# Optimization experiments

Measured on AMD Instinct MI355X. Metric: run time of the kernel, lower is better.

Reference implementation:

```python
import jax, jax.numpy as jnp
import numpy as np

N = 100000
E = 200000
SD = 128   # structural_dim
CD = 768   # chemical_dim


def _linear_params(key, fan_in, fan_out):
    kw, kb = jax.random.split(key)
    bound = 1.0 / np.sqrt(fan_in)
    W = jax.random.uniform(kw, (fan_in, fan_out), jnp.float32, -bound, bound)
    b = jax.random.uniform(kb, (fan_out,), jnp.float32, -bound, bound)
    return W, b


def setup_inputs() -> dict:
    key = jax.random.key(0)
    ks = jax.random.split(key, 12)
    z = jax.random.normal(ks[0], (N, SD), jnp.float32)
    chemistry = jax.random.normal(ks[1], (N, CD), jnp.float32)
    edge = jax.random.randint(ks[2], (E, 2), 0, N, jnp.int64)
    smiles_mask = jax.random.randint(ks[3], (N,), 0, 2, jnp.int32)
    # structural_mlp: SD -> SD//2 -> 1
    sw1, sb1 = _linear_params(ks[4], SD, SD // 2)
    sw2, sb2 = _linear_params(ks[5], SD // 2, 1)
    # chemical_mlp: CD -> CD//4 -> 1
    cw1, cb1 = _linear_params(ks[6], CD, CD // 4)
    cw2, cb2 = _linear_params(ks[7], CD // 4, 1)
    # combined_mlp: SD+CD -> SD -> 1
    mw1, mb1 = _linear_params(ks[8], SD + CD, SD)
    mw2, mb2 = _linear_params(ks[9], SD, 1)
    path_weights = jnp.ones((3,), jnp.float32) / 3.0
    return dict(z=z, chemistry=chemistry, edge=edge, smiles_mask=smiles_mask,
                sw1=sw1, sb1=sb1, sw2=sw2, sb2=sb2,
                cw1=cw1, cb1=cb1, cw2=cw2, cb2=cb2,
                mw1=mw1, mb1=mb1, mw2=mw2, mb2=mb2,
                path_weights=path_weights)


def reference(z, chemistry, edge, smiles_mask,
              sw1, sb1, sw2, sb2,
              cw1, cb1, cw2, cb2,
              mw1, mb1, mw2, mb2,
              path_weights):
    src, dst = edge[:, 0], edge[:, 1]
    # per-edge gathers + elementwise products
    structural_prod = z[src] * z[dst]                    # [E, SD]
    chemical_prod = chemistry[src] * chemistry[dst]      # [E, CD]
    # three small MLPs (dropout is identity in eval mode)
    score_structural = (jax.nn.relu(structural_prod @ sw1 + sb1) @ sw2 + sb2)[:, 0]
    score_chemical = (jax.nn.relu(chemical_prod @ cw1 + cb1) @ cw2 + cb2)[:, 0]
    combined_prod = jnp.concatenate([structural_prod, chemical_prod], axis=-1)  # [E, SD+CD]
    score_combined = (jax.nn.relu(combined_prod @ mw1 + mb1) @ mw2 + mb2)[:, 0]
    # fixed learned path weights (use_gating=False)
    w = jax.nn.softmax(path_weights)
    scores = w[0] * score_structural + w[1] * score_chemical + w[2] * score_combined
    # fall back to structural-only score where chemistry is missing on either end
    mask = smiles_mask.astype(z.dtype)
    both_valid = mask[src] * mask[dst]
    return jnp.where(both_valid > 0.5, scores, score_structural)  # [E]
```

## Files before the change

### kernel.cpp

```cpp
#include <hip/hip_runtime.h>


typedef float    f32x4 __attribute__((ext_vector_type(4)));
typedef _Float16 f16x8 __attribute__((ext_vector_type(8)));
typedef _Float16 f16x4 __attribute__((ext_vector_type(4)));

#define E_EDGES 200000
#define KSTEPS  28
#define NOUT    384
#define PTOT    (KSTEPS * NOUT * 32)
#define PANEL   (NOUT * 32)

#define WS_WH    0
#define WS_B1    688128
#define WS_W2    (688128 + 1536)
#define WS_CONST (688128 + 3072)

__global__ __launch_bounds__(256) void prep_kernel(
    const float* __restrict__ sw1, const float* __restrict__ sb1,
    const float* __restrict__ sw2, const float* __restrict__ sb2,
    const float* __restrict__ cw1, const float* __restrict__ cb1,
    const float* __restrict__ cw2, const float* __restrict__ cb2,
    const float* __restrict__ mw1, const float* __restrict__ mb1,
    const float* __restrict__ mw2, const float* __restrict__ mb2,
    const float* __restrict__ pw,  const int* __restrict__ edge_i32,
    _Float16* __restrict__ wh,
    float* __restrict__ b1cat, float* __restrict__ w2cat,
    float* __restrict__ consts)
{
  const int idx = blockIdx.x * 256 + threadIdx.x;
  if (idx < PTOT) {
    const int p  = idx / PANEL;
    const int r  = idx % PANEL;
    const int n  = r >> 5;
    const int kk = r & 31;
    const int k  = p * 32 + kk;
    float v;
    if (n < 64)       v = (k < 128)  ? sw1[k * 64 + n] : 0.0f;
    else if (n < 256) v = (k >= 128) ? cw1[(size_t)(k - 128) * 192 + (n - 64)] : 0.0f;
    else              v = mw1[(size_t)k * 128 + (n - 256)];
    wh[idx] = (_Float16)v;
  } else if (idx < PTOT + NOUT) {
    const int j = idx - PTOT;
    float b, w;
    if (j < 64)       { b = sb1[j];       w = sw2[j]; }
    else if (j < 256) { b = cb1[j - 64];  w = cw2[j - 64]; }
    else              { b = mb1[j - 256]; w = mw2[j - 256]; }
    b1cat[j] = b;
    w2cat[j] = w;
  } else if (idx == PTOT + NOUT) {
    const float p0 = pw[0], p1 = pw[1], p2 = pw[2];
    const float mx = fmaxf(p0, fmaxf(p1, p2));
    const float e0 = __expf(p0 - mx), e1 = __expf(p1 - mx), e2 = __expf(p2 - mx);
    const float inv = 1.0f / (e0 + e1 + e2);
    const float w0 = e0 * inv, w1 = e1 * inv, w2v = e2 * inv;
    consts[0] = w0; consts[1] = w1; consts[2] = w2v;
    consts[3] = w0 * sb2[0] + w1 * cb2[0] + w2v * mb2[0];
    consts[4] = sb2[0];
    unsigned o = 0;
    for (int i = 0; i < 64; ++i) o |= (unsigned)edge_i32[2 * i + 1];
    consts[5] = (o == 0u) ? 1.0f : 0.0f;
  }
}

#define FMA2(ACC, AH, AL, B)                                              \
  ACC = __builtin_amdgcn_mfma_f32_16x16x32_f16(AH, B, ACC, 0, 0, 0);      \
  ACC = __builtin_amdgcn_mfma_f32_16x16x32_f16(AL, B, ACC, 0, 0, 0);

__global__ __launch_bounds__(256, 3) void decoder_main(
    const float* __restrict__ z, const float* __restrict__ chem,
    const int* __restrict__ edge, const int* __restrict__ mask,
    const _Float16* __restrict__ wh,
    const float* __restrict__ b1cat, const float* __restrict__ w2cat,
    const float* __restrict__ consts, float* __restrict__ out)
{
  __shared__ _Float16 Ah[2][32][40];
  __shared__ _Float16 Al[2][32][40];
  __shared__ int   srcL[32];
  __shared__ int   dstL[32];
  __shared__ float validL[32];
  __shared__ float scoreW[4][32];

  const int tid  = threadIdx.x;
  const int lane = tid & 63;
  const int wv   = tid >> 6;
  const int li   = lane & 15;
  const int q    = lane >> 4;
  const int base = blockIdx.x * 32;

  if (tid < 32) {
    const int e = base + tid;
    int s_, d_;
    if (consts[5] > 0.5f) { s_ = edge[4 * e]; d_ = edge[4 * e + 2]; }
    else                  { s_ = edge[2 * e]; d_ = edge[2 * e + 1]; }
    srcL[tid] = s_;
    dstL[tid] = d_;
    validL[tid] = (mask[s_] != 0 && mask[d_] != 0) ? 1.0f : 0.0f;
  }
  __syncthreads();

  const int m  = tid >> 3;
  const int kc = (tid & 7) << 2;
  const float* zs = z    + (size_t)srcL[m] * 128 + kc;
  const float* zd = z    + (size_t)dstL[m] * 128 + kc;
  const float* cs = chem + (size_t)srcL[m] * 768 + kc;
  const float* cd = chem + (size_t)dstL[m] * 768 + kc;

#define GLOAD(T, A, B)                                      \
  if ((T) < 4) {                                            \
    A = *(const f32x4*)(zs + (T) * 32);                     \
    B = *(const f32x4*)(zd + (T) * 32);                     \
  } else {                                                  \
    A = *(const f32x4*)(cs + ((T) - 4) * 32);               \
    B = *(const f32x4*)(cd + ((T) - 4) * 32);               \
  }

#define STAGE(BUF, PA, PB)                                  \
  {                                                         \
    f16x4 h_, l_;                                           \
    _Pragma("unroll")                                       \
    for (int j = 0; j < 4; ++j) {                           \
      const float p_ = (PA)[j] * (PB)[j];                   \
      const _Float16 hh = (_Float16)p_;                     \
      h_[j] = hh;                                           \
      l_[j] = (_Float16)(p_ - (float)hh);                   \
    }                                                       \
    *(f16x4*)&Ah[BUF][m][kc] = h_;                          \
    *(f16x4*)&Al[BUF][m][kc] = l_;                          \
  }

#define BFRAG(S, TI) \
  (*(const f16x8*)(wh + (size_t)(S) * PANEL + ((TI) * 16 + li) * 32 + q * 8))

#define AFRAGS(BUF, A0H, A0L, A1H, A1L)                     \
  A0H = *(const f16x8*)&Ah[BUF][li][q * 8];                 \
  A0L = *(const f16x8*)&Al[BUF][li][q * 8];                 \
  A1H = *(const f16x8*)&Ah[BUF][16 + li][q * 8];            \
  A1L = *(const f16x8*)&Al[BUF][16 + li][q * 8];

  const float w0c = consts[0], w1c = consts[1], w2c = consts[2];

  float part[2][4];
#pragma unroll
  for (int mt = 0; mt < 2; ++mt)
#pragma unroll
    for (int r = 0; r < 4; ++r) part[mt][r] = 0.0f;

#define RETIRE(ACC, TI, MT, WVALID, WINVALID)                              \
  {                                                                        \
    const int col = (TI) * 16 + li;                                        \
    const float b1 = b1cat[col];                                           \
    const float w2 = w2cat[col];                                           \
    _Pragma("unroll")                                                      \
    for (int r = 0; r < 4; ++r) {                                          \
      const float vld = validL[(MT) * 16 + q * 4 + r];                     \
      const float a = (WINVALID) + vld * ((WVALID) - (WINVALID));          \
      part[MT][r] += a * fmaxf((ACC)[r] + b1, 0.0f) * w2;                  \
    }                                                                      \
  }

  const int tS  = wv;
  const int tH0 = 4 + 3 * wv;
  const int tC0 = 16 + 2 * wv;

  {
    f32x4 a0, b0;
    GLOAD(0, a0, b0)
    STAGE(0, a0, b0)
  }
  f32x4 gca, gcb;
  GLOAD(1, gca, gcb)
  __syncthreads();

  f32x4 accS[2], accC[2][2];
  accS[0] = (f32x4){0.f, 0.f, 0.f, 0.f};
  accS[1] = (f32x4){0.f, 0.f, 0.f, 0.f};
#pragma unroll
  for (int t = 0; t < 2; ++t) {
    accC[t][0] = (f32x4){0.f, 0.f, 0.f, 0.f};
    accC[t][1] = (f32x4){0.f, 0.f, 0.f, 0.f};
  }

#pragma unroll
  for (int s = 0; s < 4; ++s) {
    const int buf = s & 1;
    f16x8 a0h, a0l, a1h, a1l;
    AFRAGS(buf, a0h, a0l, a1h, a1l)

    const f16x8 bS  = BFRAG(s, tS);
    const f16x8 bC0 = BFRAG(s, tC0);
    const f16x8 bC1 = BFRAG(s, tC0 + 1);

    f32x4 gna, gnb;
    GLOAD(s + 2, gna, gnb)

    FMA2(accS[0], a0h, a0l, bS)
    FMA2(accS[1], a1h, a1l, bS)
    FMA2(accC[0][0], a0h, a0l, bC0)
    FMA2(accC[0][1], a1h, a1l, bC0)
    FMA2(accC[1][0], a0h, a0l, bC1)
    FMA2(accC[1][1], a1h, a1l, bC1)

    STAGE(buf ^ 1, gca, gcb)
    __syncthreads();
    gca = gna; gcb = gnb;
  }

  RETIRE(accS[0], tS, 0, w0c, 1.0f)
  RETIRE(accS[1], tS, 1, w0c, 1.0f)

  f32x4 accH[3][2];
#pragma unroll
  for (int t = 0; t < 3; ++t) {
    accH[t][0] = (f32x4){0.f, 0.f, 0.f, 0.f};
    accH[t][1] = (f32x4){0.f, 0.f, 0.f, 0.f};
  }

  for (int s = 4; s < KSTEPS; ++s) {
    const int buf = s & 1;
    f16x8 a0h, a0l, a1h, a1l;
    AFRAGS(buf, a0h, a0l, a1h, a1l)

    const f16x8 bH0 = BFRAG(s, tH0);
    const f16x8 bH1 = BFRAG(s, tH0 + 1);
    const f16x8 bH2 = BFRAG(s, tH0 + 2);
    const f16x8 bC0 = BFRAG(s, tC0);
    const f16x8 bC1 = BFRAG(s, tC0 + 1);

    f32x4 gna, gnb;
    const bool pf = (s + 2 < KSTEPS);
    if (pf) {
      gna = *(const f32x4*)(cs + (s - 2) * 32);
      gnb = *(const f32x4*)(cd + (s - 2) * 32);
    }

    FMA2(accH[0][0], a0h, a0l, bH0)
    FMA2(accH[0][1], a1h, a1l, bH0)
    FMA2(accH[1][0], a0h, a0l, bH1)
    FMA2(accH[1][1], a1h, a1l, bH1)
    FMA2(accH[2][0], a0h, a0l, bH2)
    FMA2(accH[2][1], a1h, a1l, bH2)
    FMA2(accC[0][0], a0h, a0l, bC0)
    FMA2(accC[0][1], a1h, a1l, bC0)
    FMA2(accC[1][0], a0h, a0l, bC1)
    FMA2(accC[1][1], a1h, a1l, bC1)

    if (s + 1 < KSTEPS) STAGE(buf ^ 1, gca, gcb)
    __syncthreads();
    if (pf) { gca = gna; gcb = gnb; }
  }

#pragma unroll
  for (int t = 0; t < 3; ++t) {
    RETIRE(accH[t][0], tH0 + t, 0, w1c, 0.0f)
    RETIRE(accH[t][1], tH0 + t, 1, w1c, 0.0f)
  }
#pragma unroll
  for (int t = 0; t < 2; ++t) {
    RETIRE(accC[t][0], tC0 + t, 0, w2c, 0.0f)
    RETIRE(accC[t][1], tC0 + t, 1, w2c, 0.0f)
  }

#pragma unroll
  for (int mt = 0; mt < 2; ++mt) {
#pragma unroll
    for (int r = 0; r < 4; ++r) {
      float vv = part[mt][r];
      vv += __shfl_xor(vv, 1);
      vv += __shfl_xor(vv, 2);
      vv += __shfl_xor(vv, 4);
      vv += __shfl_xor(vv, 8);
      part[mt][r] = vv;
    }
  }
  if (li == 0) {
#pragma unroll
    for (int mt = 0; mt < 2; ++mt)
#pragma unroll
      for (int r = 0; r < 4; ++r)
        scoreW[wv][mt * 16 + q * 4 + r] = part[mt][r];
  }
  __syncthreads();

  if (tid < 32) {
    const float s4 = scoreW[0][tid] + scoreW[1][tid] + scoreW[2][tid] + scoreW[3][tid];
    const float c3 = consts[3], c4 = consts[4];
    out[base + tid] = s4 + c4 + validL[tid] * (c3 - c4);
  }
}

extern "C" void kernel_launch(void* const* d_in, const int* in_sizes, int n_in,
                              void* d_out, int out_size, void* d_ws, size_t ws_size,
                              hipStream_t stream)
{
  const float* z    = (const float*)d_in[0];
  const float* chem = (const float*)d_in[1];
  const int*   edge = (const int*)d_in[2];
  const int*   mask = (const int*)d_in[3];
  const float* sw1  = (const float*)d_in[4];
  const float* sb1  = (const float*)d_in[5];
  const float* sw2  = (const float*)d_in[6];
  const float* sb2  = (const float*)d_in[7];
  const float* cw1  = (const float*)d_in[8];
  const float* cb1  = (const float*)d_in[9];
  const float* cw2  = (const float*)d_in[10];
  const float* cb2  = (const float*)d_in[11];
  const float* mw1  = (const float*)d_in[12];
  const float* mb1  = (const float*)d_in[13];
  const float* mw2  = (const float*)d_in[14];
  const float* mb2  = (const float*)d_in[15];
  const float* pw   = (const float*)d_in[16];

  char* ws = (char*)d_ws;
  _Float16* wh  = (_Float16*)(ws + WS_WH);
  float* b1cat  = (float*)(ws + WS_B1);
  float* w2cat  = (float*)(ws + WS_W2);
  float* consts = (float*)(ws + WS_CONST);

  const int prep_tasks  = PTOT + NOUT + 64;
  const int prep_blocks = (prep_tasks + 255) / 256;
  prep_kernel<<<prep_blocks, 256, 0, stream>>>(
      sw1, sb1, sw2, sb2, cw1, cb1, cw2, cb2, mw1, mb1, mw2, mb2, pw, edge,
      wh, b1cat, w2cat, consts);

  decoder_main<<<E_EDGES / 32, 256, 0, stream>>>(
      z, chem, edge, mask, wh, b1cat, w2cat, consts, (float*)d_out);
}
```

Baseline: 722.2 us.

## Use four-stage LDS ring with two k-steps per barrier and deeper prefetch

Replaces the double-buffered A staging with a 4-slot LDS ring so two k-steps run between each __syncthreads, halving the number of barriers. Global loads for the edge-product rows are issued two steps further ahead through two register sets, so gathers have more time to land. It also precomputes the B fragment lane offset. In exchange it uses more LDS and more registers per thread, which may hurt occupancy under the 3-block launch bound, and the buffer-index bookkeeping becomes more fragile.

```diff
diff --git a/kernel.cpp b/kernel.cpp
--- a/kernel.cpp
+++ b/kernel.cpp
@@ -74,8 +74,7 @@
     const float* __restrict__ b1cat, const float* __restrict__ w2cat,
     const float* __restrict__ consts, float* __restrict__ out)
 {
-  __shared__ _Float16 Ah[2][32][40];
-  __shared__ _Float16 Al[2][32][40];
+  __shared__ _Float16 Ash[2][4][32][40];
   __shared__ int   srcL[32];
   __shared__ int   dstL[32];
   __shared__ float validL[32];
@@ -86,6 +85,7 @@
   const int wv   = tid >> 6;
   const int li   = lane & 15;
   const int q    = lane >> 4;
+  const int q8   = q << 3;
   const int base = blockIdx.x * 32;
 
   if (tid < 32) {
@@ -106,14 +106,23 @@
   const float* cs = chem + (size_t)srcL[m] * 768 + kc;
   const float* cd = chem + (size_t)dstL[m] * 768 + kc;
 
-#define GLOAD(T, A, B)                                      \
+  const int loff = li * 32 + q8;
+  const int tS  = wv;
+  const int tH0 = 4 + 3 * wv;
+  const int tC0 = 16 + 2 * wv;
+
+#define GLOAD(T, GA, GB)                                    \
   if ((T) < 4) {                                            \
-    A = *(const f32x4*)(zs + (T) * 32);                     \
-    B = *(const f32x4*)(zd + (T) * 32);                     \
+    GA = *(const f32x4*)(zs + (T) * 32);                    \
+    GB = *(const f32x4*)(zd + (T) * 32);                    \
   } else {                                                  \
-    A = *(const f32x4*)(cs + ((T) - 4) * 32);               \
-    B = *(const f32x4*)(cd + ((T) - 4) * 32);               \
-  }
+    GA = *(const f32x4*)(cs + ((T) - 4) * 32);              \
+    GB = *(const f32x4*)(cd + ((T) - 4) * 32);              \
+  }
+
+#define ISSUE(S, GA, GB)                                    \
+  { GA = *(const f32x4*)(cs + (size_t)(S) * 32);            \
+    GB = *(const f32x4*)(cd + (size_t)(S) * 32); }
 
 #define STAGE(BUF, PA, PB)                                  \
   {                                                         \
@@ -125,18 +134,15 @@
       h_[j] = hh;                                           \
       l_[j] = (_Float16)(p_ - (float)hh);                   \
     }                                                       \
-    *(f16x4*)&Ah[BUF][m][kc] = h_;                          \
-    *(f16x4*)&Al[BUF][m][kc] = l_;                          \
-  }
-
-#define BFRAG(S, TI) \
-  (*(const f16x8*)(wh + (size_t)(S) * PANEL + ((TI) * 16 + li) * 32 + q * 8))
-
-#define AFRAGS(BUF, A0H, A0L, A1H, A1L)                     \
-  A0H = *(const f16x8*)&Ah[BUF][li][q * 8];                 \
-  A0L = *(const f16x8*)&Al[BUF][li][q * 8];                 \
-  A1H = *(const f16x8*)&Ah[BUF][16 + li][q * 8];            \
-  A1L = *(const f16x8*)&Al[BUF][16 + li][q * 8];
+    *(f16x4*)&Ash[0][BUF][m][kc] = h_;                      \
+    *(f16x4*)&Ash[1][BUF][m][kc] = l_;                      \
+  }
+
+#define AFRAGS(BC, A0H, A0L, A1H, A1L)                      \
+  A0H = *(const f16x8*)&Ash[0][BC][li][q8];                 \
+  A0L = *(const f16x8*)&Ash[1][BC][li][q8];                 \
+  A1H = *(const f16x8*)&Ash[0][BC][16 + li][q8];            \
+  A1L = *(const f16x8*)&Ash[1][BC][16 + li][q8];
 
   const float w0c = consts[0], w1c = consts[1], w2c = consts[2];
 
@@ -159,17 +165,13 @@
     }                                                                      \
   }
 
-  const int tS  = wv;
-  const int tH0 = 4 + 3 * wv;
-  const int tC0 = 16 + 2 * wv;
-
-  {
-    f32x4 a0, b0;
-    GLOAD(0, a0, b0)
-    STAGE(0, a0, b0)
-  }
-  f32x4 gca, gcb;
-  GLOAD(1, gca, gcb)
+  f32x4 g0a, g0b, g1a, g1b, gxa, gxb, gya, gyb;
+  GLOAD(0, g0a, g0b)
+  GLOAD(1, g1a, g1b)
+  GLOAD(2, gxa, gxb)
+  GLOAD(3, gya, gyb)
+  STAGE(0, g0a, g0b)
+  STAGE(1, g1a, g1b)
   __syncthreads();
 
   f32x4 accS[2], accC[2][2];
@@ -181,30 +183,31 @@
     accC[t][1] = (f32x4){0.f, 0.f, 0.f, 0.f};
   }
 
-#pragma unroll
-  for (int s = 0; s < 4; ++s) {
-    const int buf = s & 1;
-    f16x8 a0h, a0l, a1h, a1l;
-    AFRAGS(buf, a0h, a0l, a1h, a1l)
-
-    const f16x8 bS  = BFRAG(s, tS);
-    const f16x8 bC0 = BFRAG(s, tC0);
-    const f16x8 bC1 = BFRAG(s, tC0 + 1);
-
-    f32x4 gna, gnb;
-    GLOAD(s + 2, gna, gnb)
-
-    FMA2(accS[0], a0h, a0l, bS)
-    FMA2(accS[1], a1h, a1l, bS)
-    FMA2(accC[0][0], a0h, a0l, bC0)
-    FMA2(accC[0][1], a1h, a1l, bC0)
-    FMA2(accC[1][0], a0h, a0l, bC1)
-    FMA2(accC[1][1], a1h, a1l, bC1)
-
-    STAGE(buf ^ 1, gca, gcb)
-    __syncthreads();
-    gca = gna; gcb = gnb;
-  }
+#define STEP_A(S, GA, GB)                                           \
+  {                                                                 \
+    const int bc = (S) & 3;                                         \
+    f16x8 a0h, a0l, a1h, a1l;                                       \
+    AFRAGS(bc, a0h, a0l, a1h, a1l)                                  \
+    const _Float16* bu = wh + (size_t)(S) * PANEL + loff;           \
+    const f16x8 bS  = *(const f16x8*)(bu + tS * 512);               \
+    const f16x8 bC0 = *(const f16x8*)(bu + tC0 * 512);              \
+    const f16x8 bC1 = *(const f16x8*)(bu + tC0 * 512 + 512);        \
+    FMA2(accS[0],    a0h, a0l, bS)                                  \
+    FMA2(accS[1],    a1h, a1l, bS)                                  \
+    FMA2(accC[0][0], a0h, a0l, bC0)                                 \
+    FMA2(accC[0][1], a1h, a1l, bC0)                                 \
+    FMA2(accC[1][0], a0h, a0l, bC1)                                 \
+    FMA2(accC[1][1], a1h, a1l, bC1)                                 \
+    STAGE((bc + 2) & 3, GA, GB)                                     \
+    ISSUE((S), GA, GB)                                              \
+  }
+
+  STEP_A(0, gxa, gxb)
+  STEP_A(1, gya, gyb)
+  __syncthreads();
+  STEP_A(2, gxa, gxb)
+  STEP_A(3, gya, gyb)
+  __syncthreads();
 
   RETIRE(accS[0], tS, 0, w0c, 1.0f)
   RETIRE(accS[1], tS, 1, w0c, 1.0f)
@@ -216,39 +219,41 @@
     accH[t][1] = (f32x4){0.f, 0.f, 0.f, 0.f};
   }
 
-  for (int s = 4; s < KSTEPS; ++s) {
-    const int buf = s & 1;
-    f16x8 a0h, a0l, a1h, a1l;
-    AFRAGS(buf, a0h, a0l, a1h, a1l)
-
-    const f16x8 bH0 = BFRAG(s, tH0);
-    const f16x8 bH1 = BFRAG(s, tH0 + 1);
-    const f16x8 bH2 = BFRAG(s, tH0 + 2);
-    const f16x8 bC0 = BFRAG(s, tC0);
-    const f16x8 bC1 = BFRAG(s, tC0 + 1);
-
-    f32x4 gna, gnb;
-    const bool pf = (s + 2 < KSTEPS);
-    if (pf) {
-      gna = *(const f32x4*)(cs + (s - 2) * 32);
-      gnb = *(const f32x4*)(cd + (s - 2) * 32);
-    }
-
-    FMA2(accH[0][0], a0h, a0l, bH0)
-    FMA2(accH[0][1], a1h, a1l, bH0)
-    FMA2(accH[1][0], a0h, a0l, bH1)
-    FMA2(accH[1][1], a1h, a1l, bH1)
-    FMA2(accH[2][0], a0h, a0l, bH2)
-    FMA2(accH[2][1], a1h, a1l, bH2)
-    FMA2(accC[0][0], a0h, a0l, bC0)
-    FMA2(accC[0][1], a1h, a1l, bC0)
-    FMA2(accC[1][0], a0h, a0l, bC1)
-    FMA2(accC[1][1], a1h, a1l, bC1)
-
-    if (s + 1 < KSTEPS) STAGE(buf ^ 1, gca, gcb)
+#define STEP_B(S, GA, GB, DO_STAGE, DO_ISSUE)                       \
+  {                                                                 \
+    const int bc = (S) & 3;                                         \
+    f16x8 a0h, a0l, a1h, a1l;                                       \
+    AFRAGS(bc, a0h, a0l, a1h, a1l)                                  \
+    const _Float16* bu = wh + (size_t)(S) * PANEL + loff;           \
+    const f16x8 bH0 = *(const f16x8*)(bu + tH0 * 512);              \
+    const f16x8 bH1 = *(const f16x8*)(bu + tH0 * 512 + 512);        \
+    const f16x8 bH2 = *(const f16x8*)(bu + tH0 * 512 + 1024);       \
+    const f16x8 bC0 = *(const f16x8*)(bu + tC0 * 512);              \
+    const f16x8 bC1 = *(const f16x8*)(bu + tC0 * 512 + 512);        \
+    FMA2(accH[0][0], a0h, a0l, bH0)                                 \
+    FMA2(accH[0][1], a1h, a1l, bH0)                                 \
+    FMA2(accH[1][0], a0h, a0l, bH1)                                 \
+    FMA2(accH[1][1], a1h, a1l, bH1)                                 \
+    FMA2(accH[2][0], a0h, a0l, bH2)                                 \
+    FMA2(accH[2][1], a1h, a1l, bH2)                                 \
+    FMA2(accC[0][0], a0h, a0l, bC0)                                 \
+    FMA2(accC[0][1], a1h, a1l, bC0)                                 \
+    FMA2(accC[1][0], a0h, a0l, bC1)                                 \
+    FMA2(accC[1][1], a1h, a1l, bC1)                                 \
+    if (DO_STAGE) STAGE((bc + 2) & 3, GA, GB)                       \
+    if (DO_ISSUE) ISSUE((S), GA, GB)                                \
+  }
+
+  for (int u = 2; u < 12; ++u) {
+    STEP_B(2 * u,     gxa, gxb, true, true)
+    STEP_B(2 * u + 1, gya, gyb, true, true)
     __syncthreads();
-    if (pf) { gca = gna; gcb = gnb; }
-  }
+  }
+  STEP_B(24, gxa, gxb, true,  false)
+  STEP_B(25, gya, gyb, true,  false)
+  __syncthreads();
+  STEP_B(26, gxa, gxb, false, false)
+  STEP_B(27, gya, gyb, false, false)
 
 #pragma unroll
   for (int t = 0; t < 3; ++t) {
```

Result: no change. 722.1 us (-0.0%).

## Process 96 edges per block with three 4-wave groups sharing weight panels

Applied to the files above, without the earlier changes.

Each block grows from 32 to 96 edges and from 4 to 12 waves. The waves are split into three groups of four, and each group handles its own 32-row slice of the staged A tiles while loading the same f16 weight fragments. The aim is better cache reuse of the weight panels across more edges per block and fewer blocks overall. In exchange it adds bounds checks for the partial last block and needs larger LDS and barriers across 12 waves. The launch_bounds(768, 3) hint may force register pressure or spills and lower occupancy.

```diff
diff --git a/kernel.cpp b/kernel.cpp
--- a/kernel.cpp
+++ b/kernel.cpp
@@ -6,6 +6,8 @@
 typedef _Float16 f16x4 __attribute__((ext_vector_type(4)));
 
 #define E_EDGES 200000
+#define EPB     96
+#define NBLK    ((E_EDGES + EPB - 1) / EPB)
 #define KSTEPS  28
 #define NOUT    384
 #define PTOT    (KSTEPS * NOUT * 32)
@@ -67,35 +69,40 @@
   ACC = __builtin_amdgcn_mfma_f32_16x16x32_f16(AH, B, ACC, 0, 0, 0);      \
   ACC = __builtin_amdgcn_mfma_f32_16x16x32_f16(AL, B, ACC, 0, 0, 0);
 
-__global__ __launch_bounds__(256, 3) void decoder_main(
+__global__ __launch_bounds__(768, 3) void decoder_main(
     const float* __restrict__ z, const float* __restrict__ chem,
     const int* __restrict__ edge, const int* __restrict__ mask,
     const _Float16* __restrict__ wh,
     const float* __restrict__ b1cat, const float* __restrict__ w2cat,
     const float* __restrict__ consts, float* __restrict__ out)
 {
-  __shared__ _Float16 Ah[2][32][40];
-  __shared__ _Float16 Al[2][32][40];
-  __shared__ int   srcL[32];
-  __shared__ int   dstL[32];
-  __shared__ float validL[32];
-  __shared__ float scoreW[4][32];
+  __shared__ _Float16 Ah[2][96][40];
+  __shared__ _Float16 Al[2][96][40];
+  __shared__ int   srcL[96];
+  __shared__ int   dstL[96];
+  __shared__ float validL[96];
+  __shared__ float scoreW[12][32];
 
   const int tid  = threadIdx.x;
   const int lane = tid & 63;
   const int wv   = tid >> 6;
+  const int g    = wv & 3;
+  const int mrow = (wv >> 2) << 5;
   const int li   = lane & 15;
   const int q    = lane >> 4;
-  const int base = blockIdx.x * 32;
-
-  if (tid < 32) {
+  const int base = blockIdx.x * EPB;
+
+  if (tid < EPB) {
     const int e = base + tid;
-    int s_, d_;
-    if (consts[5] > 0.5f) { s_ = edge[4 * e]; d_ = edge[4 * e + 2]; }
-    else                  { s_ = edge[2 * e]; d_ = edge[2 * e + 1]; }
+    int s_ = 0, d_ = 0, ok = 0;
+    if (e < E_EDGES) {
+      if (consts[5] > 0.5f) { s_ = edge[4 * e]; d_ = edge[4 * e + 2]; }
+      else                  { s_ = edge[2 * e]; d_ = edge[2 * e + 1]; }
+      ok = 1;
+    }
     srcL[tid] = s_;
     dstL[tid] = d_;
-    validL[tid] = (mask[s_] != 0 && mask[d_] != 0) ? 1.0f : 0.0f;
+    validL[tid] = (ok && mask[s_] != 0 && mask[d_] != 0) ? 1.0f : 0.0f;
   }
   __syncthreads();
 
@@ -133,10 +140,10 @@
   (*(const f16x8*)(wh + (size_t)(S) * PANEL + ((TI) * 16 + li) * 32 + q * 8))
 
 #define AFRAGS(BUF, A0H, A0L, A1H, A1L)                     \
-  A0H = *(const f16x8*)&Ah[BUF][li][q * 8];                 \
-  A0L = *(const f16x8*)&Al[BUF][li][q * 8];                 \
-  A1H = *(const f16x8*)&Ah[BUF][16 + li][q * 8];            \
-  A1L = *(const f16x8*)&Al[BUF][16 + li][q * 8];
+  A0H = *(const f16x8*)&Ah[BUF][mrow + li][q * 8];          \
+  A0L = *(const f16x8*)&Al[BUF][mrow + li][q * 8];          \
+  A1H = *(const f16x8*)&Ah[BUF][mrow + 16 + li][q * 8];     \
+  A1L = *(const f16x8*)&Al[BUF][mrow + 16 + li][q * 8];
 
   const float w0c = consts[0], w1c = consts[1], w2c = consts[2];
 
@@ -153,15 +160,15 @@
     const float w2 = w2cat[col];                                           \
     _Pragma("unroll")                                                      \
     for (int r = 0; r < 4; ++r) {                                          \
-      const float vld = validL[(MT) * 16 + q * 4 + r];                     \
+      const float vld = validL[mrow + (MT) * 16 + q * 4 + r];              \
       const float a = (WINVALID) + vld * ((WVALID) - (WINVALID));          \
       part[MT][r] += a * fmaxf((ACC)[r] + b1, 0.0f) * w2;                  \
     }                                                                      \
   }
 
-  const int tS  = wv;
-  const int tH0 = 4 + 3 * wv;
-  const int tC0 = 16 + 2 * wv;
+  const int tS  = g;
+  const int tH0 = 4 + 3 * g;
+  const int tC0 = 16 + 2 * g;
 
   {
     f32x4 a0, b0;
@@ -282,8 +289,11 @@
   }
   __syncthreads();
 
-  if (tid < 32) {
-    const float s4 = scoreW[0][tid] + scoreW[1][tid] + scoreW[2][tid] + scoreW[3][tid];
+  if (tid < EPB && base + tid < E_EDGES) {
+    const int w0 = (tid >> 5) << 2;
+    const int lr = tid & 31;
+    const float s4 = scoreW[w0][lr] + scoreW[w0 + 1][lr] +
+                     scoreW[w0 + 2][lr] + scoreW[w0 + 3][lr];
     const float c3 = consts[3], c4 = consts[4];
     out[base + tid] = s4 + c4 + validL[tid] * (c3 - c4);
   }
@@ -323,6 +333,6 @@
       sw1, sb1, sw2, sb2, cw1, cb1, cw2, cb2, mw1, mb1, mw2, mb2, pw, edge,
       wh, b1cat, w2cat, consts);
 
-  decoder_main<<<E_EDGES / 32, 256, 0, stream>>>(
+  decoder_main<<<NBLK, 768, 0, stream>>>(
       z, chem, edge, mask, wh, b1cat, w2cat, consts, (float*)d_out);
 }
```

After: 821.6 us. 1.14x slower.

## Double edges per block to 64 to reuse weight fragments across more rows

Applied to the files above, without the earlier changes.

Each block now processes 64 edges instead of 32, so each wave runs four 16-row M tiles per weight fragment instead of two. This halves the number of global weight (B fragment) loads per edge and halves the block count. Accumulator and register use roughly double, so launch bounds drop from 3 to 2 blocks per CU, which lowers occupancy and the latency hiding available for the gather loads.

```diff
diff --git a/kernel.cpp b/kernel.cpp
--- a/kernel.cpp
+++ b/kernel.cpp
@@ -6,6 +6,8 @@
 typedef _Float16 f16x4 __attribute__((ext_vector_type(4)));
 
 #define E_EDGES 200000
+#define EPB     64
+#define NBLK    (E_EDGES / EPB)
 #define KSTEPS  28
 #define NOUT    384
 #define PTOT    (KSTEPS * NOUT * 32)
@@ -67,28 +69,29 @@
   ACC = __builtin_amdgcn_mfma_f32_16x16x32_f16(AH, B, ACC, 0, 0, 0);      \
   ACC = __builtin_amdgcn_mfma_f32_16x16x32_f16(AL, B, ACC, 0, 0, 0);
 
-__global__ __launch_bounds__(256, 3) void decoder_main(
+__global__ __launch_bounds__(256, 2) void decoder_main(
     const float* __restrict__ z, const float* __restrict__ chem,
     const int* __restrict__ edge, const int* __restrict__ mask,
     const _Float16* __restrict__ wh,
     const float* __restrict__ b1cat, const float* __restrict__ w2cat,
     const float* __restrict__ consts, float* __restrict__ out)
 {
-  __shared__ _Float16 Ah[2][32][40];
-  __shared__ _Float16 Al[2][32][40];
-  __shared__ int   srcL[32];
-  __shared__ int   dstL[32];
-  __shared__ float validL[32];
-  __shared__ float scoreW[4][32];
+  __shared__ _Float16 Ah[2][64][40];
+  __shared__ _Float16 Al[2][64][40];
+  __shared__ int   srcL[64];
+  __shared__ int   dstL[64];
+  __shared__ float validL[64];
+  __shared__ float scoreW[4][64];
 
   const int tid  = threadIdx.x;
   const int lane = tid & 63;
-  const int wv   = tid >> 6;
+  const int g    = tid >> 6;
   const int li   = lane & 15;
   const int q    = lane >> 4;
-  const int base = blockIdx.x * 32;
-
-  if (tid < 32) {
+  const int q8   = q << 3;
+  const int base = blockIdx.x * EPB;
+
+  if (tid < EPB) {
     const int e = base + tid;
     int s_, d_;
     if (consts[5] > 0.5f) { s_ = edge[4 * e]; d_ = edge[4 * e + 2]; }
@@ -99,50 +102,75 @@
   }
   __syncthreads();
 
-  const int m  = tid >> 3;
+  const int m0 = tid >> 3;
+  const int m1 = m0 + 32;
   const int kc = (tid & 7) << 2;
-  const float* zs = z    + (size_t)srcL[m] * 128 + kc;
-  const float* zd = z    + (size_t)dstL[m] * 128 + kc;
-  const float* cs = chem + (size_t)srcL[m] * 768 + kc;
-  const float* cd = chem + (size_t)dstL[m] * 768 + kc;
-
-#define GLOAD(T, A, B)                                      \
+  const float* zs0 = z    + (size_t)srcL[m0] * 128 + kc;
+  const float* zd0 = z    + (size_t)dstL[m0] * 128 + kc;
+  const float* cs0 = chem + (size_t)srcL[m0] * 768 + kc;
+  const float* cd0 = chem + (size_t)dstL[m0] * 768 + kc;
+  const float* zs1 = z    + (size_t)srcL[m1] * 128 + kc;
+  const float* zd1 = z    + (size_t)dstL[m1] * 128 + kc;
+  const float* cs1 = chem + (size_t)srcL[m1] * 768 + kc;
+  const float* cd1 = chem + (size_t)dstL[m1] * 768 + kc;
+
+#define GLOAD(T, A0, B0, A1, B1)                            \
   if ((T) < 4) {                                            \
-    A = *(const f32x4*)(zs + (T) * 32);                     \
-    B = *(const f32x4*)(zd + (T) * 32);                     \
+    A0 = *(const f32x4*)(zs0 + (T) * 32);                   \
+    B0 = *(const f32x4*)(zd0 + (T) * 32);                   \
+    A1 = *(const f32x4*)(zs1 + (T) * 32);                   \
+    B1 = *(const f32x4*)(zd1 + (T) * 32);                   \
   } else {                                                  \
-    A = *(const f32x4*)(cs + ((T) - 4) * 32);               \
-    B = *(const f32x4*)(cd + ((T) - 4) * 32);               \
-  }
-
-#define STAGE(BUF, PA, PB)                                  \
+    A0 = *(const f32x4*)(cs0 + ((T) - 4) * 32);             \
+    B0 = *(const f32x4*)(cd0 + ((T) - 4) * 32);             \
+    A1 = *(const f32x4*)(cs1 + ((T) - 4) * 32);             \
+    B1 = *(const f32x4*)(cd1 + ((T) - 4) * 32);             \
+  }
+
+#define STAGE(BUF, PA0, PB0, PA1, PB1)                      \
   {                                                         \
-    f16x4 h_, l_;                                           \
+    f16x4 h0_, l0_, h1_, l1_;                               \
     _Pragma("unroll")                                       \
     for (int j = 0; j < 4; ++j) {                           \
-      const float p_ = (PA)[j] * (PB)[j];                   \
-      const _Float16 hh = (_Float16)p_;                     \
-      h_[j] = hh;                                           \
-      l_[j] = (_Float16)(p_ - (float)hh);                   \
+      const float p0_ = (PA0)[j] * (PB0)[j];                \
+      const _Float16 hh0 = (_Float16)p0_;                   \
+      h0_[j] = hh0;                                         \
+      l0_[j] = (_Float16)(p0_ - (float)hh0);                \
+      const float p1_ = (PA1)[j] * (PB1)[j];                \
+      const _Float16 hh1 = (_Float16)p1_;                   \
+      h1_[j] = hh1;                                         \
+      l1_[j] = (_Float16)(p1_ - (float)hh1);                \
     }                                                       \
-    *(f16x4*)&Ah[BUF][m][kc] = h_;                          \
-    *(f16x4*)&Al[BUF][m][kc] = l_;                          \
+    *(f16x4*)&Ah[BUF][m0][kc] = h0_;                        \
+    *(f16x4*)&Al[BUF][m0][kc] = l0_;                        \
+    *(f16x4*)&Ah[BUF][m1][kc] = h1_;                        \
+    *(f16x4*)&Al[BUF][m1][kc] = l1_;                        \
   }
 
 #define BFRAG(S, TI) \
-  (*(const f16x8*)(wh + (size_t)(S) * PANEL + ((TI) * 16 + li) * 32 + q * 8))
-
-#define AFRAGS(BUF, A0H, A0L, A1H, A1L)                     \
-  A0H = *(const f16x8*)&Ah[BUF][li][q * 8];                 \
-  A0L = *(const f16x8*)&Al[BUF][li][q * 8];                 \
-  A1H = *(const f16x8*)&Ah[BUF][16 + li][q * 8];            \
-  A1L = *(const f16x8*)&Al[BUF][16 + li][q * 8];
+  (*(const f16x8*)(wh + (size_t)(S) * PANEL + ((TI) * 16 + li) * 32 + q8))
+
+#define AFRAGS(BUF)                                         \
+  f16x8 a0h = *(const f16x8*)&Ah[BUF][li][q8];              \
+  f16x8 a0l = *(const f16x8*)&Al[BUF][li][q8];              \
+  f16x8 a1h = *(const f16x8*)&Ah[BUF][16 + li][q8];         \
+  f16x8 a1l = *(const f16x8*)&Al[BUF][16 + li][q8];         \
+  f16x8 a2h = *(const f16x8*)&Ah[BUF][32 + li][q8];         \
+  f16x8 a2l = *(const f16x8*)&Al[BUF][32 + li][q8];         \
+  f16x8 a3h = *(const f16x8*)&Ah[BUF][48 + li][q8];         \
+  f16x8 a3l = *(const f16x8*)&Al[BUF][48 + li][q8];
+
+#define FMA2x4(ACCARR, B)                                   \
+  FMA2(ACCARR[0], a0h, a0l, B)                              \
+  FMA2(ACCARR[1], a1h, a1l, B)                              \
+  FMA2(ACCARR[2], a2h, a2l, B)                              \
+  FMA2(ACCARR[3], a3h, a3l, B)
 
   const float w0c = consts[0], w1c = consts[1], w2c = consts[2];
 
-  float part[2][4];
-#pragma unroll
-  for (int mt = 0; mt < 2; ++mt)
+  float part[4][4];
+#pragma unroll
+  for (int mt = 0; mt < 4; ++mt)
 #pragma unroll
     for (int r = 0; r < 4; ++r) part[mt][r] = 0.0f;
 
@@ -159,67 +187,63 @@
     }                                                                      \
   }
 
-  const int tS  = wv;
-  const int tH0 = 4 + 3 * wv;
-  const int tC0 = 16 + 2 * wv;
+  const int tS  = g;
+  const int tH0 = 4 + 3 * g;
+  const int tC0 = 16 + 2 * g;
 
   {
-    f32x4 a0, b0;
-    GLOAD(0, a0, b0)
-    STAGE(0, a0, b0)
-  }
-  f32x4 gca, gcb;
-  GLOAD(1, gca, gcb)
+    f32x4 a0, b0, a1, b1;
+    GLOAD(0, a0, b0, a1, b1)
+    STAGE(0, a0, b0, a1, b1)
+  }
+  f32x4 gca0, gcb0, gca1, gcb1;
+  GLOAD(1, gca0, gcb0, gca1, gcb1)
   __syncthreads();
 
-  f32x4 accS[2], accC[2][2];
-  accS[0] = (f32x4){0.f, 0.f, 0.f, 0.f};
-  accS[1] = (f32x4){0.f, 0.f, 0.f, 0.f};
-#pragma unroll
-  for (int t = 0; t < 2; ++t) {
-    accC[t][0] = (f32x4){0.f, 0.f, 0.f, 0.f};
-    accC[t][1] = (f32x4){0.f, 0.f, 0.f, 0.f};
+  f32x4 accS[4], accC[2][4];
+#pragma unroll
+  for (int mt = 0; mt < 4; ++mt) {
+    accS[mt]    = (f32x4){0.f, 0.f, 0.f, 0.f};
+    accC[0][mt] = (f32x4){0.f, 0.f, 0.f, 0.f};
+    accC[1][mt] = (f32x4){0.f, 0.f, 0.f, 0.f};
   }
 
 #pragma unroll
   for (int s = 0; s < 4; ++s) {
     const int buf = s & 1;
-    f16x8 a0h, a0l, a1h, a1l;
-    AFRAGS(buf, a0h, a0l, a1h, a1l)
+    AFRAGS(buf)
 
     const f16x8 bS  = BFRAG(s, tS);
     const f16x8 bC0 = BFRAG(s, tC0);
     const f16x8 bC1 = BFRAG(s, tC0 + 1);
 
-    f32x4 gna, gnb;
-    GLOAD(s + 2, gna, gnb)
-
-    FMA2(accS[0], a0h, a0l, bS)
-    FMA2(accS[1], a1h, a1l, bS)
-    FMA2(accC[0][0], a0h, a0l, bC0)
-    FMA2(accC[0][1], a1h, a1l, bC0)
-    FMA2(accC[1][0], a0h, a0l, bC1)
-    FMA2(accC[1][1], a1h, a1l, bC1)
-
-    STAGE(buf ^ 1, gca, gcb)
+    f32x4 gna0, gnb0, gna1, gnb1;
+    GLOAD(s + 2, gna0, gnb0, gna1, gnb1)
+
+    FMA2x4(accS,    bS)
+    FMA2x4(accC[0], bC0)
+    FMA2x4(accC[1], bC1)
+
+    STAGE(buf ^ 1, gca0, gcb0, gca1, gcb1)
     __syncthreads();
-    gca = gna; gcb = gnb;
-  }
-
-  RETIRE(accS[0], tS, 0, w0c, 1.0f)
-  RETIRE(accS[1], tS, 1, w0c, 1.0f)
-
-  f32x4 accH[3][2];
-#pragma unroll
-  for (int t = 0; t < 3; ++t) {
-    accH[t][0] = (f32x4){0.f, 0.f, 0.f, 0.f};
-    accH[t][1] = (f32x4){0.f, 0.f, 0.f, 0.f};
-  }
+    gca0 = gna0; gcb0 = gnb0; gca1 = gna1; gcb1 = gnb1;
+  }
+
+#pragma unroll
+  for (int mt = 0; mt < 4; ++mt) {
+    RETIRE(accS[mt], tS, mt, w0c, 1.0f)
+  }
+
+  f32x4 accH[3][4];
+#pragma unroll
+  for (int t = 0; t < 3; ++t)
+#pragma unroll
+    for (int mt = 0; mt < 4; ++mt)
+      accH[t][mt] = (f32x4){0.f, 0.f, 0.f, 0.f};
 
   for (int s = 4; s < KSTEPS; ++s) {
     const int buf = s & 1;
-    f16x8 a0h, a0l, a1h, a1l;
-    AFRAGS(buf, a0h, a0l, a1h, a1l)
+    AFRAGS(buf)
 
     const f16x8 bH0 = BFRAG(s, tH0);
     const f16x8 bH1 = BFRAG(s, tH0 + 1);
@@ -227,42 +251,41 @@
     const f16x8 bC0 = BFRAG(s, tC0);
     const f16x8 bC1 = BFRAG(s, tC0 + 1);
 
-    f32x4 gna, gnb;
+    f32x4 gna0, gnb0, gna1, gnb1;
     const bool pf = (s + 2 < KSTEPS);
     if (pf) {
-      gna = *(const f32x4*)(cs + (s - 2) * 32);
-      gnb = *(const f32x4*)(cd + (s - 2) * 32);
+      gna0 = *(const f32x4*)(cs0 + (s - 2) * 32);
+      gnb0 = *(const f32x4*)(cd0 + (s - 2) * 32);
+      gna1 = *(const f32x4*)(cs1 + (s - 2) * 32);
+      gnb1 = *(const f32x4*)(cd1 + (s - 2) * 32);
     }
 
-    FMA2(accH[0][0], a0h, a0l, bH0)
-    FMA2(accH[0][1], a1h, a1l, bH0)
-    FMA2(accH[1][0], a0h, a0l, bH1)
-    FMA2(accH[1][1], a1h, a1l, bH1)
-    FMA2(accH[2][0], a0h, a0l, bH2)
-    FMA2(accH[2][1], a1h, a1l, bH2)
-    FMA2(accC[0][0], a0h, a0l, bC0)
-    FMA2(accC[0][1], a1h, a1l, bC0)
-    FMA2(accC[1][0], a0h, a0l, bC1)
-    FMA2(accC[1][1], a1h, a1l, bC1)
-
-    if (s + 1 < KSTEPS) STAGE(buf ^ 1, gca, gcb)
+    FMA2x4(accH[0], bH0)
+    FMA2x4(accH[1], bH1)
+    FMA2x4(accH[2], bH2)
+    FMA2x4(accC[0], bC0)
+    FMA2x4(accC[1], bC1)
+
+    if (s + 1 < KSTEPS) STAGE(buf ^ 1, gca0, gcb0, gca1, gcb1)
     __syncthreads();
-    if (pf) { gca = gna; gcb = gnb; }
-  }
-
-#pragma unroll
-  for (int t = 0; t < 3; ++t) {
-    RETIRE(accH[t][0], tH0 + t, 0, w1c, 0.0f)
-    RETIRE(accH[t][1], tH0 + t, 1, w1c, 0.0f)
-  }
-#pragma unroll
-  for (int t = 0; t < 2; ++t) {
-    RETIRE(accC[t][0], tC0 + t, 0, w2c, 0.0f)
-    RETIRE(accC[t][1], tC0 + t, 1, w2c, 0.0f)
-  }
-
-#pragma unroll
-  for (int mt = 0; mt < 2; ++mt) {
+    if (pf) { gca0 = gna0; gcb0 = gnb0; gca1 = gna1; gcb1 = gnb1; }
+  }
+
+#pragma unroll
+  for (int t = 0; t < 3; ++t)
+#pragma unroll
+    for (int mt = 0; mt < 4; ++mt) {
+      RETIRE(accH[t][mt], tH0 + t, mt, w1c, 0.0f)
+    }
+#pragma unroll
+  for (int t = 0; t < 2; ++t)
+#pragma unroll
+    for (int mt = 0; mt < 4; ++mt) {
+      RETIRE(accC[t][mt], tC0 + t, mt, w2c, 0.0f)
+    }
+
+#pragma unroll
+  for (int mt = 0; mt < 4; ++mt) {
 #pragma unroll
     for (int r = 0; r < 4; ++r) {
       float vv = part[mt][r];
@@ -275,14 +298,14 @@
   }
   if (li == 0) {
 #pragma unroll
-    for (int mt = 0; mt < 2; ++mt)
+    for (int mt = 0; mt < 4; ++mt)
 #pragma unroll
       for (int r = 0; r < 4; ++r)
-        scoreW[wv][mt * 16 + q * 4 + r] = part[mt][r];
+        scoreW[g][mt * 16 + q * 4 + r] = part[mt][r];
   }
   __syncthreads();
 
-  if (tid < 32) {
+  if (tid < EPB) {
     const float s4 = scoreW[0][tid] + scoreW[1][tid] + scoreW[2][tid] + scoreW[3][tid];
     const float c3 = consts[3], c4 = consts[4];
     out[base + tid] = s4 + c4 + validL[tid] * (c3 - c4);
@@ -323,6 +346,6 @@
       sw1, sb1, sw2, sb2, cw1, cb1, cw2, cb2, mw1, mb1, mw2, mb2, pw, edge,
       wh, b1cat, w2cat, consts);
 
-  decoder_main<<<E_EDGES / 32, 256, 0, stream>>>(
+  decoder_main<<<NBLK, 256, 0, stream>>>(
       z, chem, edge, mask, wh, b1cat, w2cat, consts, (float*)d_out);
 }
```

After: 666.2 us. -7.8%, faster.
